# Performance work log

Hardware: AMD Instinct MI355X
Metric: run time of the kernel (lower is better)

## Reference

```python
import jax, jax.numpy as jnp
import numpy as np

B, L, D = 2, 2048, 2048
H, G, HD = 16, 4, 128
EPS = 1e-6
THETA_BASE = 10000.0


def setup_inputs() -> dict:
    key = jax.random.key(0)
    ks = jax.random.split(key, 5)
    x = jax.random.normal(ks[0], (B, L, D), jnp.float32)
    Wq = jax.random.normal(ks[1], (D, H * HD), jnp.float32) * 0.02
    Wk = jax.random.normal(ks[2], (D, G * HD), jnp.float32) * 0.02
    Wv = jax.random.normal(ks[3], (D, G * HD), jnp.float32) * 0.02
    Wo = jax.random.normal(ks[4], (H * HD, D), jnp.float32) * 0.02
    q_scale = jnp.ones((HD,), jnp.float32)
    k_scale = jnp.ones((HD,), jnp.float32)
    # Well-formed RoPE tables of shape [L, HD] (duplicated-half layout expected by apply_rope)
    inv_freq = 1.0 / (THETA_BASE ** (jnp.arange(0, HD // 2, dtype=jnp.float32) * 2.0 / HD))  # [HD/2]
    angles = jnp.arange(L, dtype=jnp.float32)[:, None] * inv_freq[None, :]  # [L, HD/2]
    angles = jnp.concatenate([angles, angles], axis=1)  # [L, HD]
    cos = jnp.cos(angles)
    sin = jnp.sin(angles)
    # Causal mask: True = masked (matches masked_fill(mask, -inf))
    mask = jnp.triu(jnp.ones((L, L), dtype=bool), k=1)
    return {"x": x, "Wq": Wq, "Wk": Wk, "Wv": Wv, "Wo": Wo,
            "q_scale": q_scale, "k_scale": k_scale, "cos": cos, "sin": sin, "mask": mask}


def _rmsnorm(x, scale):
    var = jnp.mean(x * x, axis=-1, keepdims=True)
    return x * jax.lax.rsqrt(var + EPS) * scale


def _rope(x, cos, sin):
    # x: [B, h, L, HD]; cos/sin: [L, HD]
    hd = x.shape[-1]
    x1, x2 = x[..., : hd // 2], x[..., hd // 2 :]
    rotated = jnp.concatenate([-x2, x1], axis=-1)
    return x * cos[None, None] + rotated * sin[None, None]


def reference(x, Wq, Wk, Wv, Wo, q_scale, k_scale, cos, sin, mask):
    b, l, _ = x.shape
    q = (x @ Wq).reshape(b, l, H, HD).transpose(0, 2, 1, 3)  # [B,H,L,HD]
    k = (x @ Wk).reshape(b, l, G, HD).transpose(0, 2, 1, 3)  # [B,G,L,HD]
    v = (x @ Wv).reshape(b, l, G, HD).transpose(0, 2, 1, 3)
    q = _rmsnorm(q, q_scale)
    k = _rmsnorm(k, k_scale)
    q = _rope(q, cos, sin)
    k = _rope(k, cos, sin)
    gs = H // G
    k = jnp.repeat(k, gs, axis=1)  # [B,H,L,HD]
    v = jnp.repeat(v, gs, axis=1)
    scores = jnp.einsum('bhqd,bhkd->bhqk', q, k)
    scores = jnp.where(mask, -jnp.inf, scores)
    # NB: faithful to the source's unusual scaling by head_dim**2 (not sqrt)
    w = jax.nn.softmax(scores / float(HD ** 2), axis=-1)
    out = jnp.einsum('bhqk,bhkd->bhqd', w, v).transpose(0, 2, 1, 3).reshape(b, l, H * HD)
    return out @ Wo
```

## Files before the change

### kernel.cpp

```cpp
#include <hip/hip_runtime.h>
#include <math.h>

#define SEQ 2048
#define DMODEL 2048
#define NHQ 16
#define NHK 4

typedef __attribute__((ext_vector_type(8))) short short8;
typedef __attribute__((ext_vector_type(8))) unsigned short ushort8;
typedef __attribute__((ext_vector_type(4))) float floatx4;

#define AS1 __attribute__((address_space(1)))
#define AS3 __attribute__((address_space(3)))

__device__ __forceinline__ unsigned short f2bf(float f) {
  unsigned int u = __builtin_bit_cast(unsigned int, f);
  u += 0x7fffu + ((u >> 16) & 1u);
  return (unsigned short)(u >> 16);
}
__device__ __forceinline__ float bf2f(unsigned short s) {
  unsigned int u = ((unsigned int)s) << 16;
  return __builtin_bit_cast(float, u);
}

__global__ __launch_bounds__(256) void prep(const float* __restrict__ x,
                                            const float* __restrict__ Wq,
                                            const float* __restrict__ Wk,
                                            const float* __restrict__ Wv,
                                            const float* __restrict__ Wo,
                                            unsigned short* __restrict__ x_bf,
                                            unsigned short* __restrict__ wqkv_t,
                                            unsigned short* __restrict__ wo_t) {
  const int z = blockIdx.z;
  const int tx = threadIdx.x, ty = threadIdx.y;
  const int tid = ty * 32 + tx;
  if (z == 3) {
    const size_t base = ((size_t)(blockIdx.y * 64 + blockIdx.x)) * 4096 + (size_t)tid * 16;
    const float4 v0 = *(const float4*)(x + base);
    const float4 v1 = *(const float4*)(x + base + 4);
    const float4 v2 = *(const float4*)(x + base + 8);
    const float4 v3 = *(const float4*)(x + base + 12);
    ushort8 w0, w1;
    w0[0] = f2bf(v0.x); w0[1] = f2bf(v0.y); w0[2] = f2bf(v0.z); w0[3] = f2bf(v0.w);
    w0[4] = f2bf(v1.x); w0[5] = f2bf(v1.y); w0[6] = f2bf(v1.z); w0[7] = f2bf(v1.w);
    w1[0] = f2bf(v2.x); w1[1] = f2bf(v2.y); w1[2] = f2bf(v2.z); w1[3] = f2bf(v2.w);
    w1[4] = f2bf(v3.x); w1[5] = f2bf(v3.y); w1[6] = f2bf(v3.z); w1[7] = f2bf(v3.w);
    *(ushort8*)(x_bf + base) = w0;
    *(ushort8*)(x_bf + base + 8) = w1;
    return;
  }
  int bx = blockIdx.x;
  const float* in;
  unsigned short* out;
  int C;
  const int R = 2048;
  if (z == 0)      { in = Wq; out = wqkv_t;                          C = 2048; }
  else if (z == 1) { in = Wo; out = wo_t;                            C = 2048; }
  else {
    if (bx < 16)      { in = Wk; out = wqkv_t + (size_t)2048 * 2048; C = 512; }
    else if (bx < 32) { in = Wv; out = wqkv_t + (size_t)2560 * 2048; C = 512; bx -= 16; }
    else return;
  }
  __shared__ float tile[32][65];
  const int c0 = bx * 32, r0 = blockIdx.y * 64;
#pragma unroll
  for (int j = 0; j < 8; ++j)
    tile[tx][ty + j * 8] = in[(size_t)(r0 + ty + j * 8) * C + c0 + tx];
  __syncthreads();
  const int c = tid >> 3;
  const int l8 = tid & 7;
  ushort8 w;
#pragma unroll
  for (int u = 0; u < 8; ++u) w[u] = f2bf(tile[c][l8 * 8 + u]);
  *(ushort8*)(out + (size_t)(c0 + c) * R + r0 + l8 * 8) = w;
}

#define PBAR() do { __builtin_amdgcn_sched_barrier(0); __builtin_amdgcn_s_barrier(); \
                    __builtin_amdgcn_sched_barrier(0); } while (0)
#define KWAIT8(deep) do { if (deep) asm volatile("s_waitcnt vmcnt(8)" ::: "memory"); \
                          else      asm volatile("s_waitcnt vmcnt(0)" ::: "memory"); } while (0)
#define KWAIT6(deep) do { if (deep) asm volatile("s_waitcnt vmcnt(6)" ::: "memory"); \
                          else      asm volatile("s_waitcnt vmcnt(0)" ::: "memory"); } while (0)

__device__ __forceinline__ void mfma_q(floatx4 (&ac)[4][4],
                                       const short8 (&a)[4], const short8 (&b)[4]) {
#pragma unroll
  for (int i = 0; i < 4; ++i)
#pragma unroll
    for (int j = 0; j < 4; ++j)
      ac[i][j] = __builtin_amdgcn_mfma_f32_16x16x32_bf16(a[i], b[j], ac[i][j], 0, 0, 0);
}

__device__ __forceinline__ void ld4(short8 (&v)[4], const unsigned short* p) {
#pragma unroll
  for (int i = 0; i < 4; ++i) v[i] = *(const short8*)(p + i * 512);
}
__device__ __forceinline__ void ld6(short8 (&v)[6], const unsigned short* p) {
#pragma unroll
  for (int i = 0; i < 6; ++i) v[i] = *(const short8*)(p + i * 512);
}

__device__ __forceinline__ void stg1(const unsigned short* src0,
                                     unsigned short* dst_uniform) {
  __builtin_amdgcn_global_load_lds((const AS1 void*)src0,
                                   (AS3 void*)dst_uniform, 16, 0, 0);
}
__device__ __forceinline__ void stg2(const unsigned short* src0,
                                     unsigned short* dst_uniform) {
  __builtin_amdgcn_global_load_lds((const AS1 void*)src0,
                                   (AS3 void*)dst_uniform, 16, 0, 0);
  __builtin_amdgcn_global_load_lds((const AS1 void*)(src0 + (size_t)128 * 2048),
                                   (AS3 void*)(dst_uniform + 4096), 16, 0, 0);
}
__device__ __forceinline__ void stg3(const unsigned short* src0,
                                     unsigned short* dst_uniform) {
  __builtin_amdgcn_global_load_lds((const AS1 void*)src0,
                                   (AS3 void*)dst_uniform, 16, 0, 0);
  __builtin_amdgcn_global_load_lds((const AS1 void*)(src0 + (size_t)128 * 2048),
                                   (AS3 void*)(dst_uniform + 4096), 16, 0, 0);
  __builtin_amdgcn_global_load_lds((const AS1 void*)(src0 + (size_t)256 * 2048),
                                   (AS3 void*)(dst_uniform + 8192), 16, 0, 0);
}

__global__ __launch_bounds__(512, 2) void gemm_qkv_fused(const unsigned short* __restrict__ A,
                                                         const unsigned short* __restrict__ Bt,
                                                         unsigned short* __restrict__ qout,
                                                         unsigned short* __restrict__ kout,
                                                         unsigned short* __restrict__ vout,
                                                         const float* __restrict__ q_scale,
                                                         const float* __restrict__ k_scale,
                                                         const float* __restrict__ cosb,
                                                         const float* __restrict__ sinb) {
  __shared__ unsigned short lds[65536];
  unsigned short* ldsA = lds;
  unsigned short* ldsB = lds + 16384;

  const int tid = threadIdx.x;
  const int wave = tid >> 6;
  const int lane = tid & 63;
  const int m15 = lane & 15;
  const int quad = lane >> 4;
  const int wr = wave >> 2;
  const int wcol = wave & 3;
  const int bxn = blockIdx.x;
  const int bm = blockIdx.y * 128;
  const int bn = bxn * 384;

  floatx4 acc[4][6];
#pragma unroll
  for (int i = 0; i < 4; ++i)
#pragma unroll
    for (int j = 0; j < 6; ++j) acc[i][j] = (floatx4){0.f, 0.f, 0.f, 0.f};

  const int srow = tid >> 2;
  const int csrc = ((tid & 3) ^ ((tid >> 3) & 3)) * 8;
  const unsigned short* gA = A + (size_t)(bm + srow) * 2048 + csrc;
  const unsigned short* gB = Bt + (size_t)(bn + srow) * 2048 + csrc;
  const int wslot = wave * 512;

  const int rc = (quad ^ ((m15 >> 1) & 3)) * 8;
  const int aoff = (wr * 64 + m15) * 32 + rc;
  const int boff = (wcol * 96 + m15) * 32 + rc;

  stg1(gA + 0,  ldsA + wslot);
  stg3(gB + 0,  ldsB + wslot);
  stg1(gA + 32, ldsA + 4096 + wslot);
  stg3(gB + 32, ldsB + 12288 + wslot);
  stg1(gA + 64, ldsA + 8192 + wslot);
  stg3(gB + 64, ldsB + 24576 + wslot);
  asm volatile("s_waitcnt vmcnt(0)" ::: "memory");
  __builtin_amdgcn_s_barrier();
  __builtin_amdgcn_sched_barrier(0);

  const int NK = 32;
  short8 af[4], bv[6];
  for (int t = 0; t < NK; ++t) {
    const int d = t & 1;
    unsigned short* Ab = ldsA + d * 8192;
    unsigned short* Bb = ldsB + d * 24576;
    unsigned short* Aalt = ldsA + (d ^ 1) * 8192;
    unsigned short* Balt = ldsB + (d ^ 1) * 24576;
    const bool st1 = (t + 1 < NK), st2 = (t + 2 < NK);
    const int k1 = (t + 1) * 64 + 32;
    const int k2 = (t + 2) * 64;

    ld4(af, Ab + aoff);
    ld6(bv, Bb + boff);
    if (st1) { stg1(gA + k1, Aalt + 4096 + wslot);
               stg3(gB + k1, Balt + 12288 + wslot); }
    PBAR();
    __builtin_amdgcn_s_setprio(1);
#pragma unroll
    for (int i = 0; i < 4; ++i)
#pragma unroll
      for (int j = 0; j < 6; ++j)
        acc[i][j] = __builtin_amdgcn_mfma_f32_16x16x32_bf16(af[i], bv[j], acc[i][j], 0, 0, 0);
    __builtin_amdgcn_s_setprio(0);
    KWAIT8(st2);
    PBAR();

    ld4(af, Ab + 4096 + aoff);
    ld6(bv, Bb + 12288 + boff);
    if (st2) { stg1(gA + k2, Ab + wslot);
               stg3(gB + k2, Bb + wslot); }
    PBAR();
    __builtin_amdgcn_s_setprio(1);
#pragma unroll
    for (int i = 0; i < 4; ++i)
#pragma unroll
      for (int j = 0; j < 6; ++j)
        acc[i][j] = __builtin_amdgcn_mfma_f32_16x16x32_bf16(af[i], bv[j], acc[i][j], 0, 0, 0);
    __builtin_amdgcn_s_setprio(0);
    KWAIT8(st2);
    PBAR();
  }

  unsigned short* epi = lds;
  const int b = bm >> 11;
  const int l_base = bm & (SEQ - 1);
  const int t64 = tid & 63;

  for (int c = 0; c < 3; ++c) {
    __syncthreads();
#pragma unroll
    for (int j = 0; j < 6; ++j) {
      const int head16 = 6 * wcol + j;
      if ((head16 >> 3) == c) {
        const int incol = (head16 & 7) * 16 + m15;
#pragma unroll
        for (int i = 0; i < 4; ++i)
#pragma unroll
          for (int r = 0; r < 4; ++r)
            epi[(wr * 64 + i * 16 + quad * 4 + r) * 129 + incol] = f2bf(acc[i][j][r]);
      }
    }
    __syncthreads();

    const int hh = 3 * bxn + c;
    if (hh < 20) {
      const float* scale = (hh < NHQ) ? q_scale : k_scale;
      unsigned short* dstbase = (hh < NHQ)
          ? qout + ((size_t)(b * NHQ + hh) * SEQ + l_base) * 128
          : kout + ((size_t)(b * NHK + (hh - NHQ)) * SEQ + l_base) * 128;
      const float sc0 = scale[t64];
      const float sc1 = scale[t64 + 64];
#pragma unroll 4
      for (int rr = 0; rr < 16; ++rr) {
        const int row = wave * 16 + rr;
        const float v0 = bf2f(epi[row * 129 + t64]);
        const float v1 = bf2f(epi[row * 129 + t64 + 64]);
        float ss = v0 * v0 + v1 * v1;
#pragma unroll
        for (int m = 1; m < 64; m <<= 1) ss += __shfl_xor(ss, m);
        const float r = rsqrtf(ss * (1.0f / 128.0f) + 1e-6f);
        const int l = l_base + row;
        const float c0v = cosb[(size_t)l * 128 + t64];
        const float s0 = sinb[(size_t)l * 128 + t64];
        const float c1v = cosb[(size_t)l * 128 + t64 + 64];
        const float s1 = sinb[(size_t)l * 128 + t64 + 64];
        const float a0 = v0 * r * sc0;
        const float a1 = v1 * r * sc1;
        unsigned short* dst = dstbase + (size_t)row * 128;
        dst[t64]      = f2bf(a0 * c0v - a1 * s0);
        dst[t64 + 64] = f2bf(a1 * c1v + a0 * s1);
      }
    } else {
      const int g = hh - 20;
      unsigned short* vbase = vout + (size_t)(b * NHK + g) * 128 * SEQ + l_base;
#pragma unroll 4
      for (int dd = 0; dd < 16; ++dd) {
        const int dcol = wave * 16 + dd;
        unsigned short* dst = vbase + (size_t)dcol * SEQ;
        dst[t64]      = epi[t64 * 129 + dcol];
        dst[t64 + 64] = epi[(t64 + 64) * 129 + dcol];
      }
    }
  }
}

__global__ __launch_bounds__(512, 2) void gemm_bf16_f32(const unsigned short* __restrict__ A,
                                                        const unsigned short* __restrict__ Bt,
                                                        float* __restrict__ C,
                                                        int M, int N, int K) {
  __shared__ unsigned short lds[49152];
  unsigned short* ldsA = lds;
  unsigned short* ldsB = lds + 16384;

  const int tid = threadIdx.x;
  const int wave = tid >> 6;
  const int lane = tid & 63;
  const int m15 = lane & 15;
  const int quad = lane >> 4;
  const int wr = wave >> 2;
  const int wcol = wave & 3;
  const int bm = blockIdx.y * 128;
  const int bn = blockIdx.x * 256;

  floatx4 acc[4][4];
#pragma unroll
  for (int i = 0; i < 4; ++i)
#pragma unroll
    for (int j = 0; j < 4; ++j) acc[i][j] = (floatx4){0.f, 0.f, 0.f, 0.f};

  const int srow = tid >> 2;
  const int csrc = ((tid & 3) ^ ((tid >> 3) & 3)) * 8;
  const unsigned short* gA = A + (size_t)(bm + srow) * 2048 + csrc;
  const unsigned short* gB = Bt + (size_t)(bn + srow) * 2048 + csrc;
  const int wslot = wave * 512;

  const int rc = (quad ^ ((m15 >> 1) & 3)) * 8;
  const int aoff = (wr * 64 + m15) * 32 + rc;
  const int boff = (wcol * 64 + m15) * 32 + rc;

  stg1(gA + 0,  ldsA + wslot);
  stg2(gB + 0,  ldsB + wslot);
  stg1(gA + 32, ldsA + 4096 + wslot);
  stg2(gB + 32, ldsB + 8192 + wslot);
  stg1(gA + 64, ldsA + 8192 + wslot);
  stg2(gB + 64, ldsB + 16384 + wslot);
  asm volatile("s_waitcnt vmcnt(0)" ::: "memory");
  __builtin_amdgcn_s_barrier();
  __builtin_amdgcn_sched_barrier(0);

  const int NK = 32;
  short8 af[4], bv[4];
  for (int t = 0; t < NK; ++t) {
    const int d = t & 1;
    unsigned short* Ab = ldsA + d * 8192;
    unsigned short* Bb = ldsB + d * 16384;
    unsigned short* Aalt = ldsA + (d ^ 1) * 8192;
    unsigned short* Balt = ldsB + (d ^ 1) * 16384;
    const bool st1 = (t + 1 < NK), st2 = (t + 2 < NK);
    const int k1 = (t + 1) * 64 + 32;
    const int k2 = (t + 2) * 64;

    ld4(af, Ab + aoff);
    ld4(bv, Bb + boff);
    if (st1) { stg1(gA + k1, Aalt + 4096 + wslot);
               stg2(gB + k1, Balt + 8192 + wslot); }
    PBAR();
    __builtin_amdgcn_s_setprio(1);
    mfma_q(acc, af, bv);
    __builtin_amdgcn_s_setprio(0);
    KWAIT6(st2);
    PBAR();

    ld4(af, Ab + 4096 + aoff);
    ld4(bv, Bb + 8192 + boff);
    if (st2) { stg1(gA + k2, Ab + wslot);
               stg2(gB + k2, Bb + wslot); }
    PBAR();
    __builtin_amdgcn_s_setprio(1);
    mfma_q(acc, af, bv);
    __builtin_amdgcn_s_setprio(0);
    KWAIT6(st2);
    PBAR();
  }

#pragma unroll
  for (int i = 0; i < 4; ++i)
#pragma unroll
    for (int j = 0; j < 4; ++j)
#pragma unroll
      for (int r = 0; r < 4; ++r) {
        const int col = bn + wcol * 64 + j * 16 + m15;
        C[(size_t)(bm + wr * 64 + i * 16 + quad * 4 + r) * N + col] = acc[i][j][r];
      }
}

__global__ __launch_bounds__(256, 4) void attn_mfma(const unsigned short* __restrict__ qb,
                                                    const unsigned short* __restrict__ kb,
                                                    const unsigned short* __restrict__ vtb,
                                                    unsigned short* __restrict__ o) {
  __shared__ unsigned short Ks[64 * 128];
  __shared__ unsigned short Vs[128 * 64];
  unsigned short* Ps = Ks;

  const int tid = threadIdx.x;
  const int wave = tid >> 6;
  const int lane = tid & 63;
  const int m15 = lane & 15;
  const int quad = lane >> 4;
  const int bh = blockIdx.x;
  const int b = bh >> 4;
  const int h = bh & 15;
  const int g = h >> 2;
  const int q0 = ((int)gridDim.y - 1 - (int)blockIdx.y) * 64;

  const unsigned short* qhead = qb + (size_t)bh * SEQ * 128;
  const unsigned short* khead = kb + (size_t)(b * NHK + g) * SEQ * 128;
  const unsigned short* vthead = vtb + (size_t)(b * NHK + g) * 128 * SEQ;

  short8 qf[4];
  {
    const unsigned short* qp = qhead + (size_t)(q0 + wave * 16 + m15) * 128 + quad * 8;
#pragma unroll
    for (int ks = 0; ks < 4; ++ks) qf[ks] = *(const short8*)(qp + ks * 32);
  }

  floatx4 acc_o[8];
#pragma unroll
  for (int n = 0; n < 8; ++n) acc_o[n] = (floatx4){0.f, 0.f, 0.f, 0.f};
  float l_lane[4] = {0.f, 0.f, 0.f, 0.f};
  const float inv_scale = 1.0f / 16384.0f;

  for (int j0 = 0; j0 <= q0; j0 += 64) {
#pragma unroll
    for (int t = 0; t < 4; ++t) {
      const int r = wave * 16 + t * 4 + (lane >> 4);
      const int cg = (lane & 15) ^ (r & 15);
      const unsigned short* src = khead + (size_t)(j0 + r) * 128 + cg * 8;
      __builtin_amdgcn_global_load_lds(
          (const AS1 void*)src,
          (AS3 void*)&Ks[(wave * 16 + t * 4) * 128], 16, 0, 0);
    }
#pragma unroll
    for (int t = 0; t < 4; ++t) {
      const int d = wave * 32 + t * 8 + (lane >> 3);
      const int cg = (lane & 7) ^ (d & 7);
      const unsigned short* src = vthead + (size_t)d * SEQ + j0 + cg * 8;
      __builtin_amdgcn_global_load_lds(
          (const AS1 void*)src,
          (AS3 void*)&Vs[(wave * 32 + t * 8) * 64], 16, 0, 0);
    }
    __syncthreads();

    floatx4 acc_s[4];
#pragma unroll
    for (int n = 0; n < 4; ++n) acc_s[n] = (floatx4){0.f, 0.f, 0.f, 0.f};
#pragma unroll
    for (int ks = 0; ks < 4; ++ks) {
#pragma unroll
      for (int n = 0; n < 4; ++n) {
        const short8 bfrag = *(const short8*)&Ks[(n * 16 + m15) * 128 + (((ks * 4 + quad) ^ m15) * 8)];
        acc_s[n] = __builtin_amdgcn_mfma_f32_16x16x32_bf16(qf[ks], bfrag, acc_s[n], 0, 0, 0);
      }
    }
    __syncthreads();

    if (j0 == q0) {
      const int row_g = wave * 16 + quad * 4;
#pragma unroll
      for (int n = 0; n < 4; ++n) {
        const int col = n * 16 + m15;
#pragma unroll
        for (int rg = 0; rg < 4; ++rg) {
          float p = (col > row_g + rg) ? 0.0f : __expf(acc_s[n][rg] * inv_scale);
          l_lane[rg] += p;
          Ps[(wave * 16 + quad * 4 + rg) * 72 + n * 16 + m15] = f2bf(p);
        }
      }
    } else {
#pragma unroll
      for (int n = 0; n < 4; ++n) {
#pragma unroll
        for (int rg = 0; rg < 4; ++rg) {
          const float p = __expf(acc_s[n][rg] * inv_scale);
          l_lane[rg] += p;
          Ps[(wave * 16 + quad * 4 + rg) * 72 + n * 16 + m15] = f2bf(p);
        }
      }
    }

#pragma unroll
    for (int kk = 0; kk < 2; ++kk) {
      const short8 a = *(const short8*)&Ps[(wave * 16 + m15) * 72 + kk * 32 + quad * 8];
#pragma unroll
      for (int n = 0; n < 8; ++n) {
        const short8 bfrag = *(const short8*)&Vs[(n * 16 + m15) * 64 + (((kk * 4 + quad) ^ (m15 & 7)) * 8)];
        acc_o[n] = __builtin_amdgcn_mfma_f32_16x16x32_bf16(a, bfrag, acc_o[n], 0, 0, 0);
      }
    }
    __syncthreads();
  }

#pragma unroll
  for (int rg = 0; rg < 4; ++rg) {
    float l = l_lane[rg];
    l += __shfl_xor(l, 1);
    l += __shfl_xor(l, 2);
    l += __shfl_xor(l, 4);
    l += __shfl_xor(l, 8);
    const float invl = 1.0f / l;
    const size_t row = (size_t)(b * SEQ + q0 + wave * 16 + quad * 4 + rg);
#pragma unroll
    for (int n = 0; n < 8; ++n)
      o[row * DMODEL + h * 128 + n * 16 + m15] = f2bf(acc_o[n][rg] * invl);
  }
}

extern "C" void kernel_launch(void* const* d_in, const int* in_sizes, int n_in,
                              void* d_out, int out_size, void* d_ws, size_t ws_size,
                              hipStream_t stream) {
  const float* x       = (const float*)d_in[0];
  const float* Wq      = (const float*)d_in[1];
  const float* Wk      = (const float*)d_in[2];
  const float* Wv      = (const float*)d_in[3];
  const float* Wo      = (const float*)d_in[4];
  const float* q_scale = (const float*)d_in[5];
  const float* k_scale = (const float*)d_in[6];
  const float* cosb    = (const float*)d_in[7];
  const float* sinb    = (const float*)d_in[8];
  float* out = (float*)d_out;

  char* w = (char*)d_ws;
  unsigned short* x_bf    = (unsigned short*)w;
  unsigned short* wqkv_t  = (unsigned short*)(w + 16777216);
  unsigned short* q_bf    = (unsigned short*)(w + 29360128);
  unsigned short* k_bf    = (unsigned short*)(w + 46137344);
  unsigned short* vt      = (unsigned short*)(w + 50331648);
  unsigned short* wo_t    = (unsigned short*)(w + 54525952);
  unsigned short* attn_bf = (unsigned short*)(w + 62914560);

  prep<<<dim3(64, 32, 4), dim3(32, 8), 0, stream>>>(x, Wq, Wk, Wv, Wo, x_bf, wqkv_t, wo_t);

  gemm_qkv_fused<<<dim3(8, 32), 512, 0, stream>>>(x_bf, wqkv_t, q_bf, k_bf, vt,
                                                  q_scale, k_scale, cosb, sinb);

  attn_mfma<<<dim3(2 * NHQ, SEQ / 64), 256, 0, stream>>>(q_bf, k_bf, vt, attn_bf);

  gemm_bf16_f32<<<dim3(2048 / 256, 4096 / 128), 512, 0, stream>>>(
      attn_bf, wo_t, out, 4096, 2048, 2048);
}
```

Measured before the change: 301.0 us.

## Process 128 query rows per attention block to reuse K/V tiles

Each attention block now covers 128 query rows instead of 64, with every wave handling two 16-row sub-tiles that share each K and V fragment read from LDS. The aim is to halve the global-to-LDS K/V traffic and the number of barriers per query row. In exchange, register use roughly doubles, launch bounds drop from 4 to 2 blocks per SM, and the grid is halved. Diagonal handling now masks across two 64-key tiles, and the shared P/K buffer grows to 128x72.

```diff
diff --git a/kernel.cpp b/kernel.cpp
--- a/kernel.cpp
+++ b/kernel.cpp
@@ -368,13 +368,14 @@
       }
 }
 
-__global__ __launch_bounds__(256, 4) void attn_mfma(const unsigned short* __restrict__ qb,
+__global__ __launch_bounds__(256, 2) void attn_mfma(const unsigned short* __restrict__ qb,
                                                     const unsigned short* __restrict__ kb,
                                                     const unsigned short* __restrict__ vtb,
                                                     unsigned short* __restrict__ o) {
-  __shared__ unsigned short Ks[64 * 128];
+  __shared__ unsigned short KsPs[128 * 72];
   __shared__ unsigned short Vs[128 * 64];
-  unsigned short* Ps = Ks;
+  unsigned short* Ks = KsPs;
+  unsigned short* Ps = KsPs;
 
   const int tid = threadIdx.x;
   const int wave = tid >> 6;
@@ -385,26 +386,30 @@
   const int b = bh >> 4;
   const int h = bh & 15;
   const int g = h >> 2;
-  const int q0 = ((int)gridDim.y - 1 - (int)blockIdx.y) * 64;
+  const int q0 = ((int)gridDim.y - 1 - (int)blockIdx.y) * 128;
 
   const unsigned short* qhead = qb + (size_t)bh * SEQ * 128;
   const unsigned short* khead = kb + (size_t)(b * NHK + g) * SEQ * 128;
   const unsigned short* vthead = vtb + (size_t)(b * NHK + g) * 128 * SEQ;
 
-  short8 qf[4];
-  {
-    const unsigned short* qp = qhead + (size_t)(q0 + wave * 16 + m15) * 128 + quad * 8;
-#pragma unroll
-    for (int ks = 0; ks < 4; ++ks) qf[ks] = *(const short8*)(qp + ks * 32);
-  }
-
-  floatx4 acc_o[8];
-#pragma unroll
-  for (int n = 0; n < 8; ++n) acc_o[n] = (floatx4){0.f, 0.f, 0.f, 0.f};
-  float l_lane[4] = {0.f, 0.f, 0.f, 0.f};
+  short8 qf[2][4];
+#pragma unroll
+  for (int r16 = 0; r16 < 2; ++r16) {
+    const unsigned short* qp =
+        qhead + (size_t)(q0 + wave * 32 + r16 * 16 + m15) * 128 + quad * 8;
+#pragma unroll
+    for (int ks = 0; ks < 4; ++ks) qf[r16][ks] = *(const short8*)(qp + ks * 32);
+  }
+
+  floatx4 acc_o[2][8];
+#pragma unroll
+  for (int r16 = 0; r16 < 2; ++r16)
+#pragma unroll
+    for (int n = 0; n < 8; ++n) acc_o[r16][n] = (floatx4){0.f, 0.f, 0.f, 0.f};
+  float l_lane[2][4] = {{0.f, 0.f, 0.f, 0.f}, {0.f, 0.f, 0.f, 0.f}};
   const float inv_scale = 1.0f / 16384.0f;
 
-  for (int j0 = 0; j0 <= q0; j0 += 64) {
+  for (int j0 = 0; j0 <= q0 + 64; j0 += 64) {
 #pragma unroll
     for (int t = 0; t < 4; ++t) {
       const int r = wave * 16 + t * 4 + (lane >> 4);
@@ -425,68 +430,80 @@
     }
     __syncthreads();
 
-    floatx4 acc_s[4];
-#pragma unroll
-    for (int n = 0; n < 4; ++n) acc_s[n] = (floatx4){0.f, 0.f, 0.f, 0.f};
+    floatx4 acc_s[2][4];
+#pragma unroll
+    for (int r16 = 0; r16 < 2; ++r16)
+#pragma unroll
+      for (int n = 0; n < 4; ++n) acc_s[r16][n] = (floatx4){0.f, 0.f, 0.f, 0.f};
 #pragma unroll
     for (int ks = 0; ks < 4; ++ks) {
 #pragma unroll
       for (int n = 0; n < 4; ++n) {
         const short8 bfrag = *(const short8*)&Ks[(n * 16 + m15) * 128 + (((ks * 4 + quad) ^ m15) * 8)];
-        acc_s[n] = __builtin_amdgcn_mfma_f32_16x16x32_bf16(qf[ks], bfrag, acc_s[n], 0, 0, 0);
+        acc_s[0][n] = __builtin_amdgcn_mfma_f32_16x16x32_bf16(qf[0][ks], bfrag, acc_s[0][n], 0, 0, 0);
+        acc_s[1][n] = __builtin_amdgcn_mfma_f32_16x16x32_bf16(qf[1][ks], bfrag, acc_s[1][n], 0, 0, 0);
       }
     }
     __syncthreads();
 
-    if (j0 == q0) {
-      const int row_g = wave * 16 + quad * 4;
-#pragma unroll
-      for (int n = 0; n < 4; ++n) {
-        const int col = n * 16 + m15;
-#pragma unroll
-        for (int rg = 0; rg < 4; ++rg) {
-          float p = (col > row_g + rg) ? 0.0f : __expf(acc_s[n][rg] * inv_scale);
-          l_lane[rg] += p;
-          Ps[(wave * 16 + quad * 4 + rg) * 72 + n * 16 + m15] = f2bf(p);
+    if (j0 >= q0) {
+#pragma unroll
+      for (int r16 = 0; r16 < 2; ++r16)
+#pragma unroll
+        for (int n = 0; n < 4; ++n) {
+#pragma unroll
+          for (int rg = 0; rg < 4; ++rg) {
+            const int row_l = wave * 32 + r16 * 16 + quad * 4 + rg;
+            const int col_l = n * 16 + m15;
+            float p = (j0 + col_l > q0 + row_l) ? 0.0f
+                                                : __expf(acc_s[r16][n][rg] * inv_scale);
+            l_lane[r16][rg] += p;
+            Ps[row_l * 72 + col_l] = f2bf(p);
+          }
         }
-      }
     } else {
 #pragma unroll
-      for (int n = 0; n < 4; ++n) {
-#pragma unroll
-        for (int rg = 0; rg < 4; ++rg) {
-          const float p = __expf(acc_s[n][rg] * inv_scale);
-          l_lane[rg] += p;
-          Ps[(wave * 16 + quad * 4 + rg) * 72 + n * 16 + m15] = f2bf(p);
+      for (int r16 = 0; r16 < 2; ++r16)
+#pragma unroll
+        for (int n = 0; n < 4; ++n) {
+#pragma unroll
+          for (int rg = 0; rg < 4; ++rg) {
+            const float p = __expf(acc_s[r16][n][rg] * inv_scale);
+            l_lane[r16][rg] += p;
+            Ps[(wave * 32 + r16 * 16 + quad * 4 + rg) * 72 + n * 16 + m15] = f2bf(p);
+          }
         }
-      }
     }
 
 #pragma unroll
     for (int kk = 0; kk < 2; ++kk) {
-      const short8 a = *(const short8*)&Ps[(wave * 16 + m15) * 72 + kk * 32 + quad * 8];
+      const short8 a0 = *(const short8*)&Ps[(wave * 32 + m15) * 72 + kk * 32 + quad * 8];
+      const short8 a1 = *(const short8*)&Ps[(wave * 32 + 16 + m15) * 72 + kk * 32 + quad * 8];
 #pragma unroll
       for (int n = 0; n < 8; ++n) {
         const short8 bfrag = *(const short8*)&Vs[(n * 16 + m15) * 64 + (((kk * 4 + quad) ^ (m15 & 7)) * 8)];
-        acc_o[n] = __builtin_amdgcn_mfma_f32_16x16x32_bf16(a, bfrag, acc_o[n], 0, 0, 0);
+        acc_o[0][n] = __builtin_amdgcn_mfma_f32_16x16x32_bf16(a0, bfrag, acc_o[0][n], 0, 0, 0);
+        acc_o[1][n] = __builtin_amdgcn_mfma_f32_16x16x32_bf16(a1, bfrag, acc_o[1][n], 0, 0, 0);
       }
     }
     __syncthreads();
   }
 
 #pragma unroll
-  for (int rg = 0; rg < 4; ++rg) {
-    float l = l_lane[rg];
-    l += __shfl_xor(l, 1);
-    l += __shfl_xor(l, 2);
-    l += __shfl_xor(l, 4);
-    l += __shfl_xor(l, 8);
-    const float invl = 1.0f / l;
-    const size_t row = (size_t)(b * SEQ + q0 + wave * 16 + quad * 4 + rg);
-#pragma unroll
-    for (int n = 0; n < 8; ++n)
-      o[row * DMODEL + h * 128 + n * 16 + m15] = f2bf(acc_o[n][rg] * invl);
-  }
+  for (int r16 = 0; r16 < 2; ++r16)
+#pragma unroll
+    for (int rg = 0; rg < 4; ++rg) {
+      float l = l_lane[r16][rg];
+      l += __shfl_xor(l, 1);
+      l += __shfl_xor(l, 2);
+      l += __shfl_xor(l, 4);
+      l += __shfl_xor(l, 8);
+      const float invl = 1.0f / l;
+      const size_t row = (size_t)(b * SEQ + q0 + wave * 32 + r16 * 16 + quad * 4 + rg);
+#pragma unroll
+      for (int n = 0; n < 8; ++n)
+        o[row * DMODEL + h * 128 + n * 16 + m15] = f2bf(acc_o[r16][n][rg] * invl);
+    }
 }
 
 extern "C" void kernel_launch(void* const* d_in, const int* in_sizes, int n_in,
@@ -517,7 +534,7 @@
   gemm_qkv_fused<<<dim3(8, 32), 512, 0, stream>>>(x_bf, wqkv_t, q_bf, k_bf, vt,
                                                   q_scale, k_scale, cosb, sinb);
 
-  attn_mfma<<<dim3(2 * NHQ, SEQ / 64), 256, 0, stream>>>(q_bf, k_bf, vt, attn_bf);
+  attn_mfma<<<dim3(2 * NHQ, SEQ / 128), 256, 0, stream>>>(q_bf, k_bf, vt, attn_bf);
 
   gemm_bf16_f32<<<dim3(2048 / 256, 4096 / 128), 512, 0, stream>>>(
       attn_bf, wo_t, out, 4096, 2048, 2048);
```

Result: slower. 310.7 us (+3.2%).
